# Kernel tuning notes

Measured on AMD Instinct MI355X. Metric: run time of the kernel, lower is better.

The kernel has to match this reference:

```python
import jax, jax.numpy as jnp
import numpy as np

D = 1024
EXPAND = 2
DI = EXPAND * D
K = 4           # d_conv
C = 64          # chunk_size
ALPHA = 0.9     # memory decay
B, S = 2, 8192
EPS = 1e-5


def setup_inputs() -> dict:
    key = jax.random.key(0)
    ks = jax.random.split(key, 10)
    s = 0.02
    return {
        "x": jax.random.normal(ks[0], (B, S, D), dtype=jnp.float32),
        "norm_w": jnp.ones((D,), dtype=jnp.float32),
        "w_up": jax.random.normal(ks[1], (D, DI), dtype=jnp.float32) * s,
        "w_gate": jax.random.normal(ks[2], (D, DI), dtype=jnp.float32) * s,
        "w_down": jax.random.normal(ks[3], (DI, D), dtype=jnp.float32) * s,
        "conv_w": jax.random.normal(ks[4], (K, 1, DI), dtype=jnp.float32) * s,  # WIO depthwise
        "conv_b": jnp.zeros((DI,), dtype=jnp.float32),
        "wq": jax.random.normal(ks[5], (D, D), dtype=jnp.float32) * s,
        "wk": jax.random.normal(ks[6], (D, D), dtype=jnp.float32) * s,
        "wv": jax.random.normal(ks[7], (D, D), dtype=jnp.float32) * s,
        "wo": jax.random.normal(ks[8], (D, D), dtype=jnp.float32) * s,
    }


def _rmsnorm(x, w):
    ms = jnp.mean(jnp.square(x.astype(jnp.float32)), axis=-1, keepdims=True)
    return (x * jax.lax.rsqrt(ms + EPS).astype(x.dtype)) * w


def _causal_depthwise_conv(u, conv_w, conv_b):
    # u: [B,S,DI]; depthwise causal conv over S, then SiLU
    y = jax.lax.conv_general_dilated(
        u, conv_w,
        window_strides=(1,), padding=[(K - 1, 0)],
        dimension_numbers=("NWC", "WIO", "NWC"),
        feature_group_count=DI)
    return jax.nn.silu(y + conv_b)


def _hebbian_memory(h, wq, wk, wv, wo):
    # chunked linear-attention style Hebbian memory
    b, s, d = h.shape
    n = s // C
    scale = d ** -0.5
    q = (h @ wq).reshape(b, n, C, d) * scale
    k = (h @ wk).reshape(b, n, C, d)
    v = (h @ wv).reshape(b, n, C, d)
    mask = jnp.tril(jnp.ones((C, C), dtype=h.dtype))  # inclusive causal within chunk

    def step(M, qkv):
        qc, kc, vc = qkv  # [b,C,d]
        inter = jnp.einsum("bcd,bde->bce", qc, M)
        attn = jnp.einsum("bcd,bed->bce", qc, kc) * mask
        intra = jnp.einsum("bce,bed->bcd", attn, vc)
        M_new = ALPHA * M + jnp.einsum("bcd,bce->bde", kc, vc)
        return M_new, inter + intra

    M0 = jnp.zeros((b, d, d), dtype=h.dtype)
    qkv = (jnp.swapaxes(q, 0, 1), jnp.swapaxes(k, 0, 1), jnp.swapaxes(v, 0, 1))
    _, o = jax.lax.scan(step, M0, qkv)        # [n,b,C,d]
    o = jnp.swapaxes(o, 0, 1).reshape(b, s, d)
    return o @ wo


def reference(x, norm_w, w_up, w_gate, w_down, conv_w, conv_b, wq, wk, wv, wo):
    normed = _rmsnorm(x, norm_w)
    val = _causal_depthwise_conv(normed @ w_up, conv_w, conv_b)   # [B,S,DI]
    gate = jax.nn.silu(normed @ w_gate)
    out = (gate * val) @ w_down                                   # [B,S,D]
    out = _hebbian_memory(out, wq, wk, wv, wo)
    return x + out
```

## Files before the change

### kernel.cpp

```cpp
#include <hip/hip_runtime.h>
#include <cstdint>
#include <cstddef>

#define SS 8192
#define DD 1024
#define DI2 2048
#define NR 16384

#define LOG2_09 (-0.152003093445050f)
#define LAMBDA16 0.185302018885184f

typedef __attribute__((ext_vector_type(4))) float f32x4;
typedef __attribute__((ext_vector_type(8))) __bf16 bf16x8;

union U16 { uint4 u; bf16x8 b; };

static __device__ __forceinline__ f32x4 MFMA(uint4 a, uint4 b, f32x4 c) {
  U16 ua, ub; ua.u = a; ub.u = b;
  return __builtin_amdgcn_mfma_f32_16x16x32_bf16(ua.b, ub.b, c, 0, 0, 0);
}

static __device__ __forceinline__ unsigned short f2bf(float f) {
  union { float f; unsigned u; } v; v.f = f;
  return (unsigned short)((v.u + 0x7FFFu + ((v.u >> 16) & 1u)) >> 16);
}
static __device__ __forceinline__ float bf2f(unsigned b) {
  union { unsigned u; float f; } v; v.u = b << 16; return v.f;
}
static __device__ __forceinline__ void unpack8(uint4 u, float* f) {
  f[0] = bf2f(u.x & 0xFFFFu); f[1] = bf2f(u.x >> 16);
  f[2] = bf2f(u.y & 0xFFFFu); f[3] = bf2f(u.y >> 16);
  f[4] = bf2f(u.z & 0xFFFFu); f[5] = bf2f(u.z >> 16);
  f[6] = bf2f(u.w & 0xFFFFu); f[7] = bf2f(u.w >> 16);
}

static __device__ __forceinline__ void glds16(const unsigned short* g, char* l) {
  __builtin_amdgcn_global_load_lds(
      (const __attribute__((address_space(1))) unsigned int*)g,
      (__attribute__((address_space(3))) unsigned int*)l, 16, 0, 0);
}

__global__ __launch_bounds__(256)
void transpose_cast(const float* __restrict__ in, unsigned short* __restrict__ out, int R, int Cc) {
  __shared__ float tile[32][33];
  const int r0 = blockIdx.y * 32, c0 = blockIdx.x * 32;
  const int tx = threadIdx.x, ty = threadIdx.y;
#pragma unroll
  for (int i = 0; i < 4; i++)
    tile[ty + i * 8][tx] = in[(size_t)(r0 + ty + i * 8) * Cc + c0 + tx];
  __syncthreads();
#pragma unroll
  for (int i = 0; i < 4; i++)
    out[(size_t)(c0 + ty + i * 8) * R + r0 + tx] = f2bf(tile[tx][ty + i * 8]);
}

__global__ __launch_bounds__(256)
void rmsnorm_kernel(const float* __restrict__ x, const float* __restrict__ w,
                    unsigned short* __restrict__ out) {
  const int row = blockIdx.x, t = threadIdx.x;
  const float4 v = ((const float4*)(x + (size_t)row * DD))[t];
  float ss = v.x * v.x + v.y * v.y + v.z * v.z + v.w * v.w;
  __shared__ float sred[256];
  sred[t] = ss;
  __syncthreads();
  for (int o = 128; o > 0; o >>= 1) {
    if (t < o) sred[t] += sred[t + o];
    __syncthreads();
  }
  const float rr = rsqrtf(sred[0] * (1.0f / (float)DD) + 1e-5f);
  const float4 wv = ((const float4*)w)[t];
  uint2 pk;
  pk.x = (unsigned)f2bf(v.x * rr * wv.x) | ((unsigned)f2bf(v.y * rr * wv.y) << 16);
  pk.y = (unsigned)f2bf(v.z * rr * wv.z) | ((unsigned)f2bf(v.w * rr * wv.w) << 16);
  *(uint2*)(out + (size_t)row * DD + t * 4) = pk;
}

enum { EP_BF16 = 0, EP_BF16_BOTH = 1, EP_BF16_T = 2, EP_F32_RES = 3, EP_STATE = 4, EP_CROSS = 5 };

template <int MODE>
__global__ __launch_bounds__(512, 2)
void gemm256(const unsigned short* __restrict__ A, const unsigned short* __restrict__ Bt,
             unsigned short* __restrict__ Cb, unsigned short* __restrict__ Ct,
             float* __restrict__ Cf, const float* __restrict__ resid,
             int M, int N, int kLen, int lda, int ldb, float scale) {
  __shared__ char sLds[131072];
  const int t = threadIdx.x, lane = t & 63, wid = t >> 6;
  const int wr = wid >> 2, wc = wid & 3;
  const int l15 = lane & 15, lh = lane >> 4;
  const int mblocks = M >> 8;
  int m0, n0;
  if ((mblocks & 7) == 0) {
    const int msl = mblocks >> 3;
    const int xcd = (int)blockIdx.x & 7, loc = (int)blockIdx.x >> 3;
    m0 = (xcd * msl + (loc % msl)) << 8;
    n0 = (loc / msl) << 8;
  } else {
    m0 = ((int)blockIdx.x % mblocks) << 8;
    n0 = ((int)blockIdx.x / mblocks) << 8;
  }
  int zb = 0, zg = 0;
  const unsigned short* Abase = A;
  const unsigned short* Bbase = Bt;
  if constexpr (MODE == EP_STATE || MODE == EP_CROSS) {
    const int gb = blockIdx.z;
    zb = gb >> 3; zg = gb & 7;
    if constexpr (MODE == EP_STATE) {
      Abase = A + (size_t)zb * DD * SS + (size_t)zg * 1024;
      Bbase = Bt + (size_t)zb * DD * SS + (size_t)zg * 1024;
    } else {
      Abase = A + ((size_t)zb * SS + (size_t)zg * 1024) * (size_t)lda;
      Bbase = Bt + ((size_t)blockIdx.z << 20);
    }
  }
  const int srow = wid * 16 + (lane >> 2);
  const int scol = ((lane & 3) << 3) ^ (((srow >> 1) & 3) << 3);
  const unsigned short* pA0 = Abase + (size_t)(m0 + srow) * lda + scol;
  const unsigned short* pA1 = pA0 + (size_t)128 * lda;
  const unsigned short* pB0 = Bbase + (size_t)(n0 + srow) * ldb + scol;
  const unsigned short* pB1 = pB0 + (size_t)128 * ldb;
  const int ldsW = wid * 1024;
  int offA[8], offB[4];
#pragma unroll
  for (int mf = 0; mf < 8; mf++) {
    const int r = wr * 128 + mf * 16 + l15;
    offA[mf] = r * 64 + ((lh * 16) ^ (((r >> 1) & 3) << 4));
  }
#pragma unroll
  for (int nf = 0; nf < 4; nf++) {
    const int r = wc * 64 + nf * 16 + l15;
    offB[nf] = r * 64 + ((lh * 16) ^ (((r >> 1) & 3) << 4));
  }
  const int NT = kLen >> 5;
#define BUFA(tt) (sLds + ((tt) & 3) * 32768)
#define BUFB(tt) (sLds + ((tt) & 3) * 32768 + 16384)
#define STAGEA(tt) do { const int _k = (tt) * 32; \
    glds16(pA0 + _k, BUFA(tt) + ldsW); \
    glds16(pA1 + _k, BUFA(tt) + 8192 + ldsW); } while (0)
#define STAGEB(tt) do { const int _k = (tt) * 32; \
    glds16(pB0 + _k, BUFB(tt) + ldsW); \
    glds16(pB1 + _k, BUFB(tt) + 8192 + ldsW); } while (0)
  STAGEA(0); STAGEB(0); STAGEA(1); STAGEB(1); STAGEA(2); STAGEB(2);
  asm volatile("s_waitcnt vmcnt(8)" ::: "memory");
  __builtin_amdgcn_s_barrier();
  f32x4 acc[8][4] = {};
  for (int kt = 0; kt < NT; ++kt) {
    const char* At  = BUFA(kt);
    const char* Bt_ = BUFB(kt);
    uint4 av[4], bv[4], av2[4];
#pragma unroll
    for (int i = 0; i < 4; i++) av[i] = *(const uint4*)(At + offA[i]);
#pragma unroll
    for (int i = 0; i < 4; i++) bv[i] = *(const uint4*)(Bt_ + offB[i]);
    if (kt + 3 < NT) STAGEA(kt + 3);
    asm volatile("s_waitcnt lgkmcnt(0)" ::: "memory");
    __builtin_amdgcn_sched_barrier(0);
    __builtin_amdgcn_s_setprio(1);
#pragma unroll
    for (int mf = 0; mf < 4; mf++)
#pragma unroll
      for (int nf = 0; nf < 4; nf++)
        acc[mf][nf] = MFMA(av[mf], bv[nf], acc[mf][nf]);
    __builtin_amdgcn_s_setprio(0);
    __builtin_amdgcn_s_barrier();
#pragma unroll
    for (int i = 0; i < 4; i++) av2[i] = *(const uint4*)(At + offA[4 + i]);
    if (kt + 3 < NT) STAGEB(kt + 3);
    asm volatile("s_waitcnt lgkmcnt(0)" ::: "memory");
    __builtin_amdgcn_sched_barrier(0);
    __builtin_amdgcn_s_setprio(1);
#pragma unroll
    for (int mf = 0; mf < 4; mf++)
#pragma unroll
      for (int nf = 0; nf < 4; nf++)
        acc[4 + mf][nf] = MFMA(av2[mf], bv[nf], acc[4 + mf][nf]);
    __builtin_amdgcn_s_setprio(0);
    if (kt < NT - 3)       { asm volatile("s_waitcnt vmcnt(8)" ::: "memory"); }
    else if (kt == NT - 3) { asm volatile("s_waitcnt vmcnt(4)" ::: "memory"); }
    else if (kt == NT - 2) { asm volatile("s_waitcnt vmcnt(0)" ::: "memory"); }
    __builtin_amdgcn_s_barrier();
  }
#undef STAGEA
#undef STAGEB
#undef BUFA
#undef BUFB
#pragma unroll
  for (int mf = 0; mf < 8; mf++) {
    const int r0 = m0 + wr * 128 + mf * 16 + lh * 4;
#pragma unroll
    for (int nf = 0; nf < 4; nf++) {
      const int c = n0 + wc * 64 + nf * 16 + l15;
      f32x4 v = acc[mf][nf] * scale;
      if constexpr (MODE == EP_F32_RES) {
#pragma unroll
        for (int jj = 0; jj < 4; jj++) {
          const size_t idx = (size_t)(r0 + jj) * N + c;
          Cf[idx] = v[jj] + resid[idx];
        }
      } else if constexpr (MODE == EP_STATE) {
        unsigned short* Tg = Cb + ((size_t)blockIdx.z << 20);
#pragma unroll
        for (int jj = 0; jj < 4; jj++)
          Tg[(size_t)(r0 + jj) * 1024 + c] = f2bf(v[jj]);
      } else if constexpr (MODE == EP_CROSS) {
        const float rs = exp2f((float)(r0 >> 6) * LOG2_09);
#pragma unroll
        for (int jj = 0; jj < 4; jj++) {
          const size_t idx = ((size_t)zb * SS + (size_t)zg * 1024 + r0 + jj) * DD + c;
          Cb[idx] = f2bf(bf2f(Cb[idx]) + v[jj] * rs);
        }
      } else {
        if constexpr (MODE == EP_BF16 || MODE == EP_BF16_BOTH) {
#pragma unroll
          for (int jj = 0; jj < 4; jj++)
            Cb[(size_t)(r0 + jj) * N + c] = f2bf(v[jj]);
        }
        if constexpr (MODE == EP_BF16_BOTH || MODE == EP_BF16_T) {
          const int bb = r0 >> 13, s0 = r0 & (SS - 1);
          float wt = 1.0f;
          if constexpr (MODE == EP_BF16_BOTH)
            wt = exp2f((float)(15 - ((s0 >> 6) & 15)) * LOG2_09);
          uint2 pk;
          pk.x = (unsigned)f2bf(v[0] * wt) | ((unsigned)f2bf(v[1] * wt) << 16);
          pk.y = (unsigned)f2bf(v[2] * wt) | ((unsigned)f2bf(v[3] * wt) << 16);
          *(uint2*)(Ct + ((size_t)bb * DD + c) * SS + s0) = pk;
        }
      }
    }
  }
}

__global__ __launch_bounds__(256)
void convgate_kernel(const unsigned short* __restrict__ ug, const float* __restrict__ cw,
                     const float* __restrict__ cb, unsigned short* __restrict__ hin) {
  const int r = blockIdx.x;
  const int c0 = threadIdx.x * 8;
  const int s = r & (SS - 1);
  float acc[8];
#pragma unroll
  for (int i = 0; i < 8; i++) acc[i] = cb[c0 + i];
  for (int tap = 0; tap < 4; tap++) {
    const int ds = s - 3 + tap;
    if (ds < 0) continue;
    uint4 uv = *(const uint4*)(ug + (size_t)(r - 3 + tap) * 4096 + c0);
    float u[8]; unpack8(uv, u);
#pragma unroll
    for (int i = 0; i < 8; i++) acc[i] += u[i] * cw[tap * DI2 + c0 + i];
  }
  uint4 gv = *(const uint4*)(ug + (size_t)r * 4096 + DI2 + c0);
  float gt[8]; unpack8(gv, gt);
  unsigned short o16[8];
#pragma unroll
  for (int i = 0; i < 8; i++) {
    const float val = acc[i] / (1.0f + __expf(-acc[i]));
    const float gg  = gt[i] / (1.0f + __expf(-gt[i]));
    o16[i] = f2bf(val * gg);
  }
  uint4 ov;
  ov.x = (unsigned)o16[0] | ((unsigned)o16[1] << 16);
  ov.y = (unsigned)o16[2] | ((unsigned)o16[3] << 16);
  ov.z = (unsigned)o16[4] | ((unsigned)o16[5] << 16);
  ov.w = (unsigned)o16[6] | ((unsigned)o16[7] << 16);
  *(uint4*)(hin + (size_t)r * DI2 + c0) = ov;
}

__global__ __launch_bounds__(256)
void prefix_kernel(unsigned short* __restrict__ Tb) {
  const int tid = blockIdx.x * 256 + threadIdx.x;
  const int b = tid >> 17, i = tid & 131071;
  unsigned short* p = Tb + (((size_t)b * 8) << 20) + (size_t)i * 8;
  float acc[8] = {};
  for (int g = 0; g < 8; g++) {
    unsigned short* pg = p + ((size_t)g << 20);
    uint4 tv = *(uint4*)pg;
    float tf_[8]; unpack8(tv, tf_);
    uint4 ov;
    ov.x = (unsigned)f2bf(acc[0]) | ((unsigned)f2bf(acc[1]) << 16);
    ov.y = (unsigned)f2bf(acc[2]) | ((unsigned)f2bf(acc[3]) << 16);
    ov.z = (unsigned)f2bf(acc[4]) | ((unsigned)f2bf(acc[5]) << 16);
    ov.w = (unsigned)f2bf(acc[6]) | ((unsigned)f2bf(acc[7]) << 16);
    *(uint4*)pg = ov;
#pragma unroll
    for (int e = 0; e < 8; e++) acc[e] = LAMBDA16 * acc[e] + tf_[e];
  }
}

__global__ __launch_bounds__(256)
void score_attn(const unsigned short* __restrict__ q, const unsigned short* __restrict__ k,
                unsigned short* __restrict__ sbuf) {
  __shared__ char sQ[4096];
  __shared__ char sK[4096];
  const int p = blockIdx.x, gb = blockIdx.y;
  int qt = (int)((sqrtf(8.0f * p + 1.0f) - 1.0f) * 0.5f);
  while ((qt + 1) * (qt + 2) / 2 <= p) qt++;
  while (qt * (qt + 1) / 2 > p) qt--;
  const int tb = p - qt * (qt + 1) / 2;
  const int b = gb >> 3, g = gb & 7;
  const int t = threadIdx.x, lane = t & 63, wid = t >> 6;
  const int l15 = lane & 15, lh = lane >> 4;
  const int srow = wid * 16 + (lane >> 2), scol = (lane & 3) * 8;
  const unsigned short* qg = q + (size_t)(b * SS + g * 1024 + qt * 64 + srow) * DD + scol;
  const unsigned short* kg = k + (size_t)(b * SS + g * 1024 + tb * 64 + srow) * DD + scol;
  char* lQ = sQ + wid * 1024;
  char* lK = sK + wid * 1024;
  f32x4 s[4] = {};
  for (int k0 = 0; k0 < DD; k0 += 32) {
    glds16(qg + k0, lQ);
    glds16(kg + k0, lK);
    __syncthreads();
    uint4 aq = *(uint4*)(sQ + (wid * 16 + l15) * 64 + lh * 16);
#pragma unroll
    for (int tf = 0; tf < 4; tf++) {
      uint4 bk = *(uint4*)(sK + (tf * 16 + l15) * 64 + lh * 16);
      s[tf] = MFMA(aq, bk, s[tf]);
    }
    __syncthreads();
  }
  const bool diag = (tb == qt);
  const float w = diag ? 1.0f : exp2f((float)(qt - 1 - tb) * LOG2_09);
  unsigned short* sb = sbuf + ((size_t)(gb * 16 + qt) * 64) * 1024 + tb * 64;
#pragma unroll
  for (int tf = 0; tf < 4; tf++)
#pragma unroll
    for (int jj = 0; jj < 4; jj++) {
      const int qr = wid * 16 + lh * 4 + jj;
      const int tc = tf * 16 + l15;
      float val = s[tf][jj] * w;
      if (diag && tc > qr) val = 0.0f;
      sb[(size_t)qr * 1024 + tc] = f2bf(val);
    }
}

__global__ __launch_bounds__(256)
void pv_attn(const unsigned short* __restrict__ sbuf, const unsigned short* __restrict__ vt,
             unsigned short* __restrict__ obuf) {
  __shared__ char sA[4096];
  __shared__ char sB[8192];
  const int et = blockIdx.x, qt = blockIdx.y, gb = blockIdx.z;
  const int b = gb >> 3, g = gb & 7;
  const int t = threadIdx.x, lane = t & 63, wid = t >> 6;
  const int l15 = lane & 15, lh = lane >> 4;
  const int srow = wid * 16 + (lane >> 2), scol = (lane & 3) * 8;
  const int e0 = et * 128;
  const unsigned short* Ag = sbuf + ((size_t)(gb * 16 + qt) * 64 + srow) * 1024 + scol;
  const unsigned short* Bg0 = vt + ((size_t)b * DD + e0 + srow) * SS + g * 1024 + scol;
  const unsigned short* Bg1 = Bg0 + (size_t)64 * SS;
  char* lA  = sA + wid * 1024;
  char* lB0 = sB + wid * 1024;
  char* lB1 = sB + 4096 + wid * 1024;
  const int tEnd = (qt + 1) * 64;
  f32x4 o[4][2] = {};
  for (int t0 = 0; t0 < tEnd; t0 += 32) {
    glds16(Ag + t0, lA);
    glds16(Bg0 + t0, lB0);
    glds16(Bg1 + t0, lB1);
    __syncthreads();
    uint4 af[4], vf[2];
#pragma unroll
    for (int mf = 0; mf < 4; mf++) af[mf] = *(uint4*)(sA + (mf * 16 + l15) * 64 + lh * 16);
#pragma unroll
    for (int nf = 0; nf < 2; nf++) vf[nf] = *(uint4*)(sB + (wid * 32 + nf * 16 + l15) * 64 + lh * 16);
#pragma unroll
    for (int mf = 0; mf < 4; mf++)
#pragma unroll
      for (int nf = 0; nf < 2; nf++)
        o[mf][nf] = MFMA(af[mf], vf[nf], o[mf][nf]);
    __syncthreads();
  }
  const size_t qrow0 = (size_t)b * SS + (size_t)g * 1024 + (size_t)qt * 64;
#pragma unroll
  for (int mf = 0; mf < 4; mf++)
#pragma unroll
    for (int nf = 0; nf < 2; nf++)
#pragma unroll
      for (int jj = 0; jj < 4; jj++)
        obuf[(qrow0 + mf * 16 + lh * 4 + jj) * DD + e0 + wid * 32 + nf * 16 + l15] =
            f2bf(o[mf][nf][jj]);
}

extern "C" void kernel_launch(void* const* d_in, const int* in_sizes, int n_in,
                              void* d_out, int out_size, void* d_ws, size_t ws_size,
                              hipStream_t stream) {
  (void)in_sizes; (void)n_in; (void)out_size;
  const float* x      = (const float*)d_in[0];
  const float* norm_w = (const float*)d_in[1];
  const float* w_up   = (const float*)d_in[2];
  const float* w_gate = (const float*)d_in[3];
  const float* w_down = (const float*)d_in[4];
  const float* conv_w = (const float*)d_in[5];
  const float* conv_b = (const float*)d_in[6];
  const float* wq     = (const float*)d_in[7];
  const float* wk     = (const float*)d_in[8];
  const float* wv     = (const float*)d_in[9];
  const float* wo     = (const float*)d_in[10];
  float* out = (float*)d_out;

  const size_t MB = 1ull << 20;
  if (ws_size < 212 * MB) return;
  char* base = (char*)d_ws;
  unsigned short* ug     = (unsigned short*)(base + 0);
  unsigned short* hbuf   = (unsigned short*)(base + 0);
  unsigned short* Tbuf   = (unsigned short*)(base + 0);
  unsigned short* qbuf   = (unsigned short*)(base + 32 * MB);
  unsigned short* kbuf   = (unsigned short*)(base + 64 * MB);
  unsigned short* ktbuf  = (unsigned short*)(base + 96 * MB);
  unsigned short* sbuf   = (unsigned short*)(base + 96 * MB);
  unsigned short* normed = (unsigned short*)(base + 128 * MB);
  unsigned short* hin    = (unsigned short*)(base + 128 * MB);
  unsigned short* vtbuf  = (unsigned short*)(base + 128 * MB);
  unsigned short* obuf   = (unsigned short*)(base + 160 * MB);
  unsigned short* wugt   = (unsigned short*)(base + 192 * MB);
  unsigned short* wdt    = (unsigned short*)(base + 200 * MB);
  unsigned short* wqt    = (unsigned short*)(base + 204 * MB);
  unsigned short* wkt    = (unsigned short*)(base + 206 * MB);
  unsigned short* wvt    = (unsigned short*)(base + 208 * MB);
  unsigned short* wot    = (unsigned short*)(base + 210 * MB);

  dim3 tb(32, 8);
  transpose_cast<<<dim3(DI2 / 32, DD / 32), tb, 0, stream>>>(w_up,   wugt,                    DD,  DI2);
  transpose_cast<<<dim3(DI2 / 32, DD / 32), tb, 0, stream>>>(w_gate, wugt + (size_t)DI2 * DD, DD,  DI2);
  transpose_cast<<<dim3(DD / 32, DI2 / 32), tb, 0, stream>>>(w_down, wdt, DI2, DD);
  transpose_cast<<<dim3(DD / 32, DD / 32),  tb, 0, stream>>>(wq, wqt, DD, DD);
  transpose_cast<<<dim3(DD / 32, DD / 32),  tb, 0, stream>>>(wk, wkt, DD, DD);
  transpose_cast<<<dim3(DD / 32, DD / 32),  tb, 0, stream>>>(wv, wvt, DD, DD);
  transpose_cast<<<dim3(DD / 32, DD / 32),  tb, 0, stream>>>(wo, wot, DD, DD);

  rmsnorm_kernel<<<NR, 256, 0, stream>>>(x, norm_w, normed);

  gemm256<EP_BF16><<<dim3((NR / 256) * (4096 / 256)), 512, 0, stream>>>(
      normed, wugt, ug, nullptr, nullptr, nullptr, NR, 4096, DD, DD, DD, 1.0f);

  convgate_kernel<<<NR, 256, 0, stream>>>(ug, conv_w, conv_b, hin);

  gemm256<EP_BF16><<<dim3((NR / 256) * (DD / 256)), 512, 0, stream>>>(
      hin, wdt, hbuf, nullptr, nullptr, nullptr, NR, DD, DI2, DI2, DI2, 1.0f);

  gemm256<EP_BF16><<<dim3((NR / 256) * (DD / 256)), 512, 0, stream>>>(
      hbuf, wqt, qbuf, nullptr, nullptr, nullptr, NR, DD, DD, DD, DD, 0.03125f);
  gemm256<EP_BF16_BOTH><<<dim3((NR / 256) * (DD / 256)), 512, 0, stream>>>(
      hbuf, wkt, kbuf, ktbuf, nullptr, nullptr, NR, DD, DD, DD, DD, 1.0f);
  gemm256<EP_BF16_T><<<dim3((NR / 256) * (DD / 256)), 512, 0, stream>>>(
      hbuf, wvt, nullptr, vtbuf, nullptr, nullptr, NR, DD, DD, DD, DD, 1.0f);

  gemm256<EP_STATE><<<dim3(16, 1, 16), 512, 0, stream>>>(
      vtbuf, ktbuf, Tbuf, nullptr, nullptr, nullptr, 1024, 1024, 1024, SS, SS, 1.0f);
  score_attn<<<dim3(136, 16), 256, 0, stream>>>(qbuf, kbuf, sbuf);
  prefix_kernel<<<1024, 256, 0, stream>>>(Tbuf);
  pv_attn<<<dim3(8, 16, 16), 256, 0, stream>>>(sbuf, vtbuf, obuf);
  gemm256<EP_CROSS><<<dim3(16, 1, 16), 512, 0, stream>>>(
      qbuf, Tbuf, obuf, nullptr, nullptr, nullptr, 1024, 1024, 1024, DD, 1024, 1.0f);

  gemm256<EP_F32_RES><<<dim3((NR / 256) * (DD / 256)), 512, 0, stream>>>(
      obuf, wot, nullptr, nullptr, out, x, NR, DD, DD, DD, DD, 1.0f);
}
```

Before: 732.9 us.

## Run intra-chunk score and PV products through the tuned 256-tile GEMM kernel

```diff
diff --git a/kernel.cpp b/kernel.cpp
--- a/kernel.cpp
+++ b/kernel.cpp
@@ -75,7 +75,8 @@
   *(uint2*)(out + (size_t)row * DD + t * 4) = pk;
 }
 
-enum { EP_BF16 = 0, EP_BF16_BOTH = 1, EP_BF16_T = 2, EP_F32_RES = 3, EP_STATE = 4, EP_CROSS = 5 };
+enum { EP_BF16 = 0, EP_BF16_BOTH = 1, EP_BF16_T = 2, EP_F32_RES = 3, EP_STATE = 4,
+       EP_CROSS = 5, EP_SCORE = 6, EP_PV = 7 };
 
 template <int MODE>
 __global__ __launch_bounds__(512, 2)
@@ -89,7 +90,12 @@
   const int l15 = lane & 15, lh = lane >> 4;
   const int mblocks = M >> 8;
   int m0, n0;
-  if ((mblocks & 7) == 0) {
+  if constexpr (MODE == EP_SCORE) {
+    const int p = (int)blockIdx.x;
+    const int mt = (p >= 6) ? 3 : (p >= 3) ? 2 : (p >= 1) ? 1 : 0;
+    const int nt = p - ((mt * (mt + 1)) >> 1);
+    m0 = mt << 8; n0 = nt << 8;
+  } else if ((mblocks & 7) == 0) {
     const int msl = mblocks >> 3;
     const int xcd = (int)blockIdx.x & 7, loc = (int)blockIdx.x >> 3;
     m0 = (xcd * msl + (loc % msl)) << 8;
@@ -101,15 +107,21 @@
   int zb = 0, zg = 0;
   const unsigned short* Abase = A;
   const unsigned short* Bbase = Bt;
-  if constexpr (MODE == EP_STATE || MODE == EP_CROSS) {
+  if constexpr (MODE == EP_STATE || MODE == EP_CROSS || MODE == EP_SCORE || MODE == EP_PV) {
     const int gb = blockIdx.z;
     zb = gb >> 3; zg = gb & 7;
     if constexpr (MODE == EP_STATE) {
       Abase = A + (size_t)zb * DD * SS + (size_t)zg * 1024;
       Bbase = Bt + (size_t)zb * DD * SS + (size_t)zg * 1024;
-    } else {
+    } else if constexpr (MODE == EP_CROSS) {
       Abase = A + ((size_t)zb * SS + (size_t)zg * 1024) * (size_t)lda;
       Bbase = Bt + ((size_t)blockIdx.z << 20);
+    } else if constexpr (MODE == EP_SCORE) {
+      Abase = A + ((size_t)zb * SS + (size_t)zg * 1024) * (size_t)lda;
+      Bbase = Bt + ((size_t)zb * SS + (size_t)zg * 1024) * (size_t)ldb;
+    } else {
+      Abase = A + ((size_t)blockIdx.z << 20);
+      Bbase = Bt + (size_t)zb * DD * SS + (size_t)zg * 1024;
     }
   }
   const int srow = wid * 16 + (lane >> 2);
@@ -130,7 +142,8 @@
     const int r = wc * 64 + nf * 16 + l15;
     offB[nf] = r * 64 + ((lh * 16) ^ (((r >> 1) & 3) << 4));
   }
-  const int NT = kLen >> 5;
+  int NT = kLen >> 5;
+  if constexpr (MODE == EP_PV) NT = ((m0 >> 8) + 1) << 3;
 #define BUFA(tt) (sLds + ((tt) & 3) * 32768)
 #define BUFB(tt) (sLds + ((tt) & 3) * 32768 + 16384)
 #define STAGEA(tt) do { const int _k = (tt) * 32; \
@@ -152,8 +165,6 @@
 #pragma unroll
     for (int i = 0; i < 4; i++) bv[i] = *(const uint4*)(Bt_ + offB[i]);
     if (kt + 3 < NT) STAGEA(kt + 3);
-    asm volatile("s_waitcnt lgkmcnt(0)" ::: "memory");
-    __builtin_amdgcn_sched_barrier(0);
     __builtin_amdgcn_s_setprio(1);
 #pragma unroll
     for (int mf = 0; mf < 4; mf++)
@@ -165,8 +176,6 @@
 #pragma unroll
     for (int i = 0; i < 4; i++) av2[i] = *(const uint4*)(At + offA[4 + i]);
     if (kt + 3 < NT) STAGEB(kt + 3);
-    asm volatile("s_waitcnt lgkmcnt(0)" ::: "memory");
-    __builtin_amdgcn_sched_barrier(0);
     __builtin_amdgcn_s_setprio(1);
 #pragma unroll
     for (int mf = 0; mf < 4; mf++)
@@ -208,6 +217,24 @@
           const size_t idx = ((size_t)zb * SS + (size_t)zg * 1024 + r0 + jj) * DD + c;
           Cb[idx] = f2bf(bf2f(Cb[idx]) + v[jj] * rs);
         }
+      } else if constexpr (MODE == EP_SCORE) {
+        unsigned short* Sg = Cb + ((size_t)blockIdx.z << 20);
+        const int qt = r0 >> 6;
+        const int tb = c >> 6;
+        float w;
+        if (tb > qt)       w = 0.0f;
+        else if (tb == qt) w = 1.0f;
+        else               w = exp2f((float)(qt - 1 - tb) * LOG2_09);
+#pragma unroll
+        for (int jj = 0; jj < 4; jj++) {
+          float val = v[jj] * w;
+          if (tb == qt && (c & 63) > ((r0 + jj) & 63)) val = 0.0f;
+          Sg[(size_t)(r0 + jj) * 1024 + c] = f2bf(val);
+        }
+      } else if constexpr (MODE == EP_PV) {
+#pragma unroll
+        for (int jj = 0; jj < 4; jj++)
+          Cb[((size_t)zb * SS + (size_t)zg * 1024 + r0 + jj) * DD + c] = f2bf(v[jj]);
       } else {
         if constexpr (MODE == EP_BF16 || MODE == EP_BF16_BOTH) {
 #pragma unroll
@@ -282,99 +309,6 @@
 #pragma unroll
     for (int e = 0; e < 8; e++) acc[e] = LAMBDA16 * acc[e] + tf_[e];
   }
-}
-
-__global__ __launch_bounds__(256)
-void score_attn(const unsigned short* __restrict__ q, const unsigned short* __restrict__ k,
-                unsigned short* __restrict__ sbuf) {
-  __shared__ char sQ[4096];
-  __shared__ char sK[4096];
-  const int p = blockIdx.x, gb = blockIdx.y;
-  int qt = (int)((sqrtf(8.0f * p + 1.0f) - 1.0f) * 0.5f);
-  while ((qt + 1) * (qt + 2) / 2 <= p) qt++;
-  while (qt * (qt + 1) / 2 > p) qt--;
-  const int tb = p - qt * (qt + 1) / 2;
-  const int b = gb >> 3, g = gb & 7;
-  const int t = threadIdx.x, lane = t & 63, wid = t >> 6;
-  const int l15 = lane & 15, lh = lane >> 4;
-  const int srow = wid * 16 + (lane >> 2), scol = (lane & 3) * 8;
-  const unsigned short* qg = q + (size_t)(b * SS + g * 1024 + qt * 64 + srow) * DD + scol;
-  const unsigned short* kg = k + (size_t)(b * SS + g * 1024 + tb * 64 + srow) * DD + scol;
-  char* lQ = sQ + wid * 1024;
-  char* lK = sK + wid * 1024;
-  f32x4 s[4] = {};
-  for (int k0 = 0; k0 < DD; k0 += 32) {
-    glds16(qg + k0, lQ);
-    glds16(kg + k0, lK);
-    __syncthreads();
-    uint4 aq = *(uint4*)(sQ + (wid * 16 + l15) * 64 + lh * 16);
-#pragma unroll
-    for (int tf = 0; tf < 4; tf++) {
-      uint4 bk = *(uint4*)(sK + (tf * 16 + l15) * 64 + lh * 16);
-      s[tf] = MFMA(aq, bk, s[tf]);
-    }
-    __syncthreads();
-  }
-  const bool diag = (tb == qt);
-  const float w = diag ? 1.0f : exp2f((float)(qt - 1 - tb) * LOG2_09);
-  unsigned short* sb = sbuf + ((size_t)(gb * 16 + qt) * 64) * 1024 + tb * 64;
-#pragma unroll
-  for (int tf = 0; tf < 4; tf++)
-#pragma unroll
-    for (int jj = 0; jj < 4; jj++) {
-      const int qr = wid * 16 + lh * 4 + jj;
-      const int tc = tf * 16 + l15;
-      float val = s[tf][jj] * w;
-      if (diag && tc > qr) val = 0.0f;
-      sb[(size_t)qr * 1024 + tc] = f2bf(val);
-    }
-}
-
-__global__ __launch_bounds__(256)
-void pv_attn(const unsigned short* __restrict__ sbuf, const unsigned short* __restrict__ vt,
-             unsigned short* __restrict__ obuf) {
-  __shared__ char sA[4096];
-  __shared__ char sB[8192];
-  const int et = blockIdx.x, qt = blockIdx.y, gb = blockIdx.z;
-  const int b = gb >> 3, g = gb & 7;
-  const int t = threadIdx.x, lane = t & 63, wid = t >> 6;
-  const int l15 = lane & 15, lh = lane >> 4;
-  const int srow = wid * 16 + (lane >> 2), scol = (lane & 3) * 8;
-  const int e0 = et * 128;
-  const unsigned short* Ag = sbuf + ((size_t)(gb * 16 + qt) * 64 + srow) * 1024 + scol;
-  const unsigned short* Bg0 = vt + ((size_t)b * DD + e0 + srow) * SS + g * 1024 + scol;
-  const unsigned short* Bg1 = Bg0 + (size_t)64 * SS;
-  char* lA  = sA + wid * 1024;
-  char* lB0 = sB + wid * 1024;
-  char* lB1 = sB + 4096 + wid * 1024;
-  const int tEnd = (qt + 1) * 64;
-  f32x4 o[4][2] = {};
-  for (int t0 = 0; t0 < tEnd; t0 += 32) {
-    glds16(Ag + t0, lA);
-    glds16(Bg0 + t0, lB0);
-    glds16(Bg1 + t0, lB1);
-    __syncthreads();
-    uint4 af[4], vf[2];
-#pragma unroll
-    for (int mf = 0; mf < 4; mf++) af[mf] = *(uint4*)(sA + (mf * 16 + l15) * 64 + lh * 16);
-#pragma unroll
-    for (int nf = 0; nf < 2; nf++) vf[nf] = *(uint4*)(sB + (wid * 32 + nf * 16 + l15) * 64 + lh * 16);
-#pragma unroll
-    for (int mf = 0; mf < 4; mf++)
-#pragma unroll
-      for (int nf = 0; nf < 2; nf++)
-        o[mf][nf] = MFMA(af[mf], vf[nf], o[mf][nf]);
-    __syncthreads();
-  }
-  const size_t qrow0 = (size_t)b * SS + (size_t)g * 1024 + (size_t)qt * 64;
-#pragma unroll
-  for (int mf = 0; mf < 4; mf++)
-#pragma unroll
-    for (int nf = 0; nf < 2; nf++)
-#pragma unroll
-      for (int jj = 0; jj < 4; jj++)
-        obuf[(qrow0 + mf * 16 + lh * 4 + jj) * DD + e0 + wid * 32 + nf * 16 + l15] =
-            f2bf(o[mf][nf][jj]);
 }
 
 extern "C" void kernel_launch(void* const* d_in, const int* in_sizes, int n_in,
@@ -443,9 +377,11 @@
 
   gemm256<EP_STATE><<<dim3(16, 1, 16), 512, 0, stream>>>(
       vtbuf, ktbuf, Tbuf, nullptr, nullptr, nullptr, 1024, 1024, 1024, SS, SS, 1.0f);
-  score_attn<<<dim3(136, 16), 256, 0, stream>>>(qbuf, kbuf, sbuf);
+  gemm256<EP_SCORE><<<dim3(10, 1, 16), 512, 0, stream>>>(
+      qbuf, kbuf, sbuf, nullptr, nullptr, nullptr, 1024, 1024, 1024, DD, DD, 1.0f);
   prefix_kernel<<<1024, 256, 0, stream>>>(Tbuf);
-  pv_attn<<<dim3(8, 16, 16), 256, 0, stream>>>(sbuf, vtbuf, obuf);
+  gemm256<EP_PV><<<dim3(16, 1, 16), 512, 0, stream>>>(
+      sbuf, vtbuf, obuf, nullptr, nullptr, nullptr, 1024, 1024, 1024, 1024, SS, 1.0f);
   gemm256<EP_CROSS><<<dim3(16, 1, 16), 512, 0, stream>>>(
       qbuf, Tbuf, obuf, nullptr, nullptr, nullptr, 1024, 1024, 1024, DD, 1024, 1.0f);
 
```

After: 697.3 us. 1.05x faster.
